# Performance work log

Hardware: AMD Instinct MI355X
Metric: run time of the kernel (lower is better)

## Reference

```python
import jax, jax.numpy as jnp
from jax import lax
import numpy as np

TOP_K = 2
CAPACITY_FACTOR = 1.0


def setup_inputs() -> dict:
    key = jax.random.key(0)
    kx, kg, k1, k2 = jax.random.split(key, 4)
    B, S, D, F, E = 8, 4096, 512, 1024, 16
    x = jax.random.normal(kx, (B, S, D), dtype=jnp.float32)
    w_gate = jax.random.normal(kg, (D, E), dtype=jnp.float32) * 0.02
    w1 = jax.random.normal(k1, (E, D, 2 * F), dtype=jnp.float32) * 0.02
    w2 = jax.random.normal(k2, (E, F, D), dtype=jnp.float32) * 0.02
    return {"x": x, "w_gate": w_gate, "w1": w1, "w2": w2}


def reference(x, w_gate, w1, w2):
    # Inference mode: no gating noise, dropout is identity.
    B, S, D = x.shape
    E = w_gate.shape[1]
    T = B * S
    capacity = max(1, int(CAPACITY_FACTOR * T / E))  # static

    flat = x.reshape(T, D)
    gate_logits = flat @ w_gate                      # [T, E]
    gate_scores = jax.nn.softmax(gate_logits, axis=-1)
    topk_vals, topk_idx = lax.top_k(gate_scores, TOP_K)  # [T, k]

    phi_mean = gate_scores.mean(axis=0)
    aux_loss = E * jnp.sum(phi_mean * phi_mean)

    # Per-expert combine weight for every token: [E, T]
    onehot = topk_idx[None, :, :] == jnp.arange(E)[:, None, None]  # [E, T, k]
    w_et = jnp.sum(jnp.where(onehot, topk_vals[None], 0.0), axis=-1)  # [E, T]

    # Capacity truncation: keep the `capacity` highest-weight tokens per expert
    sel_w, sel_idx = lax.top_k(w_et, capacity)  # [E, C]; unrouted picks have weight 0

    xs = flat[sel_idx]                                  # [E, C, D] gather
    h = jnp.einsum('ecd,edf->ecf', xs, w1)              # [E, C, 2F]
    h1, h2 = jnp.split(h, 2, axis=-1)
    act = h1 * jax.nn.silu(h2)                          # SwiGLU
    out_e = jnp.einsum('ecf,efd->ecd', act, w2) * sel_w[..., None]  # [E, C, D]

    combined = jnp.zeros((T, D), dtype=flat.dtype).at[sel_idx.reshape(-1)].add(
        out_e.reshape(-1, D))
    return combined.reshape(B, S, D), aux_loss
```

## Files before the change

### kernel.cpp

```cpp
#include <hip/hip_runtime.h>
#include <hip/hip_bf16.h>
#include <math.h>

#define T_TOK 32768
#define D_DIM 512
#define E_EXP 16
#define F_DIM 1024
#define C_CAP 2048

typedef __attribute__((ext_vector_type(8))) __bf16 bf16x8;
typedef __attribute__((ext_vector_type(4))) float f32x4;

__device__ __forceinline__ unsigned short f2bf(float f) {
  unsigned u = __float_as_uint(f);
  u += 0x7FFFu + ((u >> 16) & 1u);
  return (unsigned short)(u >> 16);
}

__device__ __forceinline__ void gld16(const void* gptr, void* ldsptr) {
  __builtin_amdgcn_global_load_lds(
      (__attribute__((address_space(1))) void*)(void*)gptr,
      (__attribute__((address_space(3))) void*)ldsptr, 16, 0, 0);
}

__global__ void transpose_conv_kernel(const float* __restrict__ in,
                                      unsigned short* __restrict__ out,
                                      int R, int Cc) {
  __shared__ float tile[32][33];
  int e = blockIdx.z;
  int r0 = blockIdx.y * 32, c0 = blockIdx.x * 32;
  const float* pin = in + (size_t)e * R * Cc;
  unsigned short* pout = out + (size_t)e * R * Cc;
  int tx = threadIdx.x, ty = threadIdx.y;
  #pragma unroll
  for (int i = 0; i < 32; i += 8)
    tile[ty + i][tx] = pin[(size_t)(r0 + ty + i) * Cc + c0 + tx];
  __syncthreads();
  #pragma unroll
  for (int i = 0; i < 32; i += 8)
    pout[(size_t)(c0 + ty + i) * R + r0 + tx] = f2bf(tile[tx][ty + i]);
}

__global__ __launch_bounds__(256) void gate_kernel(
    const float* __restrict__ x, const float* __restrict__ wg,
    float* __restrict__ w_et, float* __restrict__ phi_sum,
    unsigned short* __restrict__ xb) {
  __shared__ float wgl[D_DIM * E_EXP];
  __shared__ float phil[E_EXP];
  int tid = threadIdx.x;
  for (int i = tid; i < D_DIM * E_EXP; i += 256) wgl[i] = wg[i];
  if (tid < E_EXP) phil[tid] = 0.f;
  __syncthreads();

  int g = tid >> 4;
  int e = tid & 15;
  int t = blockIdx.x * 16 + g;

  float acc = 0.f;
  const float* xr = x + (size_t)t * D_DIM;
  #pragma unroll 4
  for (int d = 0; d < D_DIM; d += 4) {
    float4 xv = *(const float4*)(xr + d);
    acc = fmaf(xv.x, wgl[(d + 0) * 16 + e], acc);
    acc = fmaf(xv.y, wgl[(d + 1) * 16 + e], acc);
    acc = fmaf(xv.z, wgl[(d + 2) * 16 + e], acc);
    acc = fmaf(xv.w, wgl[(d + 3) * 16 + e], acc);
  }

  unsigned short* xrow = xb + (size_t)t * D_DIM;
  #pragma unroll
  for (int j = 0; j < 8; ++j) {
    int idx = j * 16 + e;
    float4 v = *(const float4*)(xr + idx * 4);
    ushort4 o;
    o.x = f2bf(v.x); o.y = f2bf(v.y); o.z = f2bf(v.z); o.w = f2bf(v.w);
    ((ushort4*)xrow)[idx] = o;
  }

  float m = acc;
  for (int off = 8; off; off >>= 1) m = fmaxf(m, __shfl_xor(m, off));
  float p = expf(acc - m);
  float s = p;
  for (int off = 8; off; off >>= 1) s += __shfl_xor(s, off);
  float score = p / s;
  atomicAdd(&phil[e], score);

  float v1 = score; int i1 = e;
  for (int off = 8; off; off >>= 1) {
    float ov = __shfl_xor(v1, off); int oi = __shfl_xor(i1, off);
    if (ov > v1 || (ov == v1 && oi < i1)) { v1 = ov; i1 = oi; }
  }
  float sc2 = (e == i1) ? -1.f : score;
  float v2 = sc2; int i2 = e;
  for (int off = 8; off; off >>= 1) {
    float ov = __shfl_xor(v2, off); int oi = __shfl_xor(i2, off);
    if (ov > v2 || (ov == v2 && oi < i2)) { v2 = ov; i2 = oi; }
  }
  if (e == 0) {
    w_et[(size_t)i1 * T_TOK + t] = v1;
    w_et[(size_t)i2 * T_TOK + t] = v2;
  }
  __syncthreads();
  if (tid < E_EXP) atomicAdd(&phi_sum[tid], phil[tid]);
}

__global__ void aux_kernel(const float* __restrict__ phi_sum, float* __restrict__ out_aux) {
  if (threadIdx.x == 0) {
    float s = 0.f;
    for (int e = 0; e < E_EXP; ++e) {
      float pm = phi_sum[e] / (float)T_TOK;
      s += pm * pm;
    }
    *out_aux = (float)E_EXP * s;
  }
}

template<int P>
__global__ __launch_bounds__(256) void s_hist(
    const float* __restrict__ w_et, unsigned* __restrict__ hist,
    const unsigned* __restrict__ prefix, const unsigned* __restrict__ done) {
  int c = blockIdx.x, e = blockIdx.y, tid = threadIdx.x;
  if (P > 0 && done[e]) return;
  __shared__ unsigned lh[2048];
  for (int i = tid; i < 2048; i += 256) lh[i] = 0;
  __syncthreads();
  const float* w = w_et + (size_t)e * T_TOK + c * 2048;
  unsigned pfx = (P > 0) ? prefix[e] : 0u;
  #pragma unroll
  for (int i = 0; i < 8; ++i) {
    unsigned b = __float_as_uint(w[i * 256 + tid]);
    if (P == 0) { if (b) atomicAdd(&lh[b >> 21], 1u); }
    else if (P == 1) { if ((b >> 21) == (pfx >> 21)) atomicAdd(&lh[(b >> 10) & 0x7FFu], 1u); }
    else { if ((b >> 10) == (pfx >> 10)) atomicAdd(&lh[b & 0x3FFu], 1u); }
  }
  __syncthreads();
  for (int i = tid; i < 2048; i += 256)
    if (lh[i]) atomicAdd(&hist[e * 2048 + i], lh[i]);
}

template<int P>
__global__ __launch_bounds__(1024) void s_pick(
    const unsigned* __restrict__ hist, unsigned* __restrict__ prefix,
    unsigned* __restrict__ krem, unsigned* __restrict__ done) {
  int tid = threadIdx.x, lane = tid & 63, e = tid >> 6;
  if (P > 0 && done[e]) return;
  const int BPL = (P == 2) ? 16 : 32;
  const int SH = (P == 0) ? 21 : (P == 1) ? 10 : 0;
  const unsigned* h = hist + e * 2048;
  unsigned S = 0;
  for (int i = 0; i < BPL; ++i) S += h[lane * BPL + i];
  unsigned U = S;
  #pragma unroll
  for (int off = 1; off < 64; off <<= 1) {
    unsigned t = __shfl_down(U, off);
    if (lane + off < 64) U += t;
  }
  unsigned Unext = __shfl_down(U, 1);
  if (lane == 63) Unext = 0;
  unsigned k = (P == 0) ? (unsigned)C_CAP : krem[e];
  if (P == 0 && lane == 0) {
    if (U < k) { done[e] = 1; prefix[e] = 0; krem[e] = 0; }
    else done[e] = 0;
  }
  if (U >= k && Unext < k) {
    unsigned cum = Unext; int chosen = 0; unsigned knew = 0;
    for (int i = BPL - 1; i >= 0; --i) {
      unsigned hh = h[lane * BPL + i];
      if (cum + hh >= k) { chosen = lane * BPL + i; knew = k - cum; break; }
      cum += hh;
    }
    if (P == 0) prefix[e] = ((unsigned)chosen) << SH;
    else prefix[e] = prefix[e] | (((unsigned)chosen) << SH);
    krem[e] = knew;
  }
}

__global__ __launch_bounds__(256) void s_count(
    const float* __restrict__ w_et, const unsigned* __restrict__ prefix,
    unsigned* __restrict__ cnt) {
  int c = blockIdx.x, e = blockIdx.y, tid = threadIdx.x;
  unsigned thr = prefix[e];
  const uint4* up = (const uint4*)(w_et + (size_t)e * T_TOK + c * 2048 + tid * 8);
  uint4 va = up[0], vb = up[1];
  unsigned gt = 0, eq = 0;
  unsigned vals[8] = {va.x, va.y, va.z, va.w, vb.x, vb.y, vb.z, vb.w};
  #pragma unroll
  for (int i = 0; i < 8; ++i) {
    if (vals[i] > thr) gt++;
    else if (vals[i] == thr) eq++;
  }
  __shared__ unsigned sc[256];
  sc[tid] = (gt << 16) | eq;
  __syncthreads();
  for (int s = 128; s; s >>= 1) {
    if (tid < s) sc[tid] += sc[tid + s];
    __syncthreads();
  }
  if (tid == 0) cnt[e * 16 + c] = sc[0];
}

__global__ __launch_bounds__(64) void s_base(
    const unsigned* __restrict__ cnt, unsigned* __restrict__ gbase,
    unsigned* __restrict__ ebase, unsigned* __restrict__ gtt,
    unsigned* __restrict__ eqt) {
  int e = threadIdx.x;
  if (e >= 16) return;
  unsigned g = 0, q = 0;
  #pragma unroll
  for (int c = 0; c < 16; ++c) {
    unsigned p = cnt[e * 16 + c];
    gbase[e * 16 + c] = g;
    ebase[e * 16 + c] = q;
    g += p >> 16;
    q += p & 0xFFFFu;
  }
  gtt[e] = g;
  eqt[e] = (unsigned)C_CAP - g;
}

__global__ __launch_bounds__(256) void s_write(
    const float* __restrict__ w_et, const unsigned* __restrict__ prefix,
    const unsigned* __restrict__ gbase, const unsigned* __restrict__ ebase,
    const unsigned* __restrict__ gtt, const unsigned* __restrict__ eqt,
    int* __restrict__ sel_idx, float* __restrict__ sel_w) {
  int c = blockIdx.x, e = blockIdx.y, tid = threadIdx.x;
  unsigned thr = prefix[e];
  const uint4* up = (const uint4*)(w_et + (size_t)e * T_TOK + c * 2048 + tid * 8);
  uint4 va = up[0], vb = up[1];
  unsigned vals[8] = {va.x, va.y, va.z, va.w, vb.x, vb.y, vb.z, vb.w};
  unsigned gt = 0, eq = 0;
  #pragma unroll
  for (int i = 0; i < 8; ++i) {
    if (vals[i] > thr) gt++;
    else if (vals[i] == thr) eq++;
  }
  __shared__ unsigned sc[256];
  unsigned mine = (gt << 16) | eq;
  sc[tid] = mine;
  __syncthreads();
  for (int off = 1; off < 256; off <<= 1) {
    unsigned add = (tid >= off) ? sc[tid - off] : 0u;
    __syncthreads();
    sc[tid] += add;
    __syncthreads();
  }
  unsigned excl = sc[tid] - mine;
  unsigned gpos = gbase[e * 16 + c] + (excl >> 16);
  unsigned qpos = ebase[e * 16 + c] + (excl & 0xFFFFu);
  unsigned gtotal = gtt[e], eqtake = eqt[e];
  int* si = sel_idx + (size_t)e * C_CAP;
  float* sw = sel_w + (size_t)e * C_CAP;
  int tokbase = c * 2048 + tid * 8;
  #pragma unroll
  for (int i = 0; i < 8; ++i) {
    unsigned b = vals[i];
    if (b > thr) {
      si[gpos] = tokbase + i; sw[gpos] = __uint_as_float(b); gpos++;
    } else if (b == thr && qpos < eqtake) {
      si[gtotal + qpos] = tokbase + i; sw[gtotal + qpos] = __uint_as_float(b); qpos++;
    }
  }
}


#define PIPE_BARRIER() do { __builtin_amdgcn_s_barrier(); __builtin_amdgcn_sched_barrier(0); } while (0)

__global__ __launch_bounds__(256, 3) void gemm1_kernel(
    const unsigned short* __restrict__ xb,
    const unsigned short* __restrict__ w1t,
    const int* __restrict__ sel_idx,
    unsigned short* __restrict__ act) {
  __shared__ __align__(16) unsigned short As[3 * 4096];
  __shared__ __align__(16) unsigned short Bs[3 * 4096];
  int bid = (blockIdx.x & 7) * 512 + (blockIdx.x >> 3);
  int nt = bid & 15, mt = (bid >> 4) & 15, e = bid >> 8;
  int tid = threadIdx.x, lane = tid & 63, wid = tid >> 6;
  int wr = wid >> 1, wc = wid & 1;
  int cl = lane & 15, rg = lane >> 4;

  int c0 = tid, c1 = 256 + tid;
  int r0 = c0 >> 2, gk0 = (c0 & 3) ^ ((r0 >> 1) & 3);
  int r1 = c1 >> 2, gk1 = (c1 & 3) ^ ((r1 >> 1) & 3);
  int tok0 = sel_idx[e * C_CAP + mt * 128 + r0];
  int tok1 = sel_idx[e * C_CAP + mt * 128 + r1];
  const unsigned short* ag0 = xb + (size_t)tok0 * D_DIM + gk0 * 8;
  const unsigned short* ag1 = xb + (size_t)tok1 * D_DIM + gk1 * 8;
  int hcol0 = (r0 < 64) ? (nt * 64 + r0) : (F_DIM + nt * 64 + (r0 - 64));
  int hcol1 = (r1 < 64) ? (nt * 64 + r1) : (F_DIM + nt * 64 + (r1 - 64));
  const unsigned short* bg0 = w1t + ((size_t)e * 2 * F_DIM + hcol0) * D_DIM + gk0 * 8;
  const unsigned short* bg1 = w1t + ((size_t)e * 2 * F_DIM + hcol1) * D_DIM + gk1 * 8;
  char* Ab = (char*)As;
  char* Bb = (char*)Bs;

#define G1_STAGE(buf, kt) do { \
    gld16(ag0 + (kt) * 32, Ab + (buf) * 8192 + tid * 16); \
    gld16(ag1 + (kt) * 32, Ab + (buf) * 8192 + 4096 + tid * 16); \
    gld16(bg0 + (kt) * 32, Bb + (buf) * 8192 + tid * 16); \
    gld16(bg1 + (kt) * 32, Bb + (buf) * 8192 + 4096 + tid * 16); \
  } while (0)

  f32x4 zero = {0.f, 0.f, 0.f, 0.f};
  f32x4 acc[4][4];
  #pragma unroll
  for (int m = 0; m < 4; ++m)
    #pragma unroll
    for (int n = 0; n < 4; ++n) acc[m][n] = zero;

#define G1_COMPUTE(buf) do { \
    const unsigned short* Ap = As + (buf) * 4096; \
    const unsigned short* Bp = Bs + (buf) * 4096; \
    bf16x8 av[4], bv[4]; \
    _Pragma("unroll") \
    for (int m = 0; m < 4; ++m) { \
      int ra = wr * 64 + m * 16 + cl; \
      av[m] = *(const bf16x8*)&Ap[(ra * 4 + (rg ^ ((ra >> 1) & 3))) * 8]; \
    } \
    _Pragma("unroll") \
    for (int n = 0; n < 4; ++n) { \
      int rb = ((n < 2) ? (wc * 32 + n * 16) : (64 + wc * 32 + (n - 2) * 16)) + cl; \
      bv[n] = *(const bf16x8*)&Bp[(rb * 4 + (rg ^ ((rb >> 1) & 3))) * 8]; \
    } \
    _Pragma("unroll") \
    for (int m = 0; m < 4; ++m) \
      _Pragma("unroll") \
      for (int n = 0; n < 4; ++n) \
        acc[m][n] = __builtin_amdgcn_mfma_f32_16x16x32_bf16(av[m], bv[n], acc[m][n], 0, 0, 0); \
  } while (0)

  const int NK = D_DIM / 32;
  G1_STAGE(0, 0);
  G1_STAGE(1, 1);
  int bc = 0, bs = 2;
  for (int kt = 0; kt < NK - 1; ++kt) {
    asm volatile("s_waitcnt vmcnt(4)" ::: "memory");
    PIPE_BARRIER();
    if (kt + 2 < NK) { G1_STAGE(bs, kt + 2); bs = (bs == 2) ? 0 : bs + 1; }
    __builtin_amdgcn_sched_barrier(0);
    G1_COMPUTE(bc);
    bc = (bc == 2) ? 0 : bc + 1;
  }
  asm volatile("s_waitcnt vmcnt(0)" ::: "memory");
  PIPE_BARRIER();
  G1_COMPUTE(bc);

  #pragma unroll
  for (int m = 0; m < 4; ++m) {
    #pragma unroll
    for (int n = 0; n < 2; ++n) {
      #pragma unroll
      for (int r = 0; r < 4; ++r) {
        int row = mt * 128 + wr * 64 + m * 16 + rg * 4 + r;
        int col = nt * 64 + wc * 32 + n * 16 + cl;
        float h1 = acc[m][n][r];
        float h2 = acc[m][n + 2][r];
        float sg = h2 / (1.f + __expf(-h2));
        act[((size_t)e * C_CAP + row) * F_DIM + col] = f2bf(h1 * sg);
      }
    }
  }
#undef G1_STAGE
#undef G1_COMPUTE
}

__global__ __launch_bounds__(256, 3) void gemm2_kernel(
    const unsigned short* __restrict__ act,
    const unsigned short* __restrict__ w2t,
    const int* __restrict__ sel_idx,
    const float* __restrict__ sel_w,
    float* __restrict__ out) {
  __shared__ __align__(16) unsigned short As[3 * 4096];
  __shared__ __align__(16) unsigned short Bs[3 * 4096];
  int bid = (blockIdx.x & 7) * 128 + (blockIdx.x >> 3);
  int nt = bid & 3, mt = (bid >> 2) & 15, e = bid >> 6;
  int tid = threadIdx.x, lane = tid & 63, wid = tid >> 6;
  int wr = wid >> 1, wc = wid & 1;
  int cl = lane & 15, rg = lane >> 4;

  int c0 = tid, c1 = 256 + tid;
  int r0 = c0 >> 2, gk0 = (c0 & 3) ^ ((r0 >> 1) & 3);
  int r1 = c1 >> 2, gk1 = (c1 & 3) ^ ((r1 >> 1) & 3);
  const unsigned short* ag0 = act + ((size_t)e * C_CAP + mt * 128 + r0) * F_DIM + gk0 * 8;
  const unsigned short* ag1 = act + ((size_t)e * C_CAP + mt * 128 + r1) * F_DIM + gk1 * 8;
  const unsigned short* bg0 = w2t + ((size_t)e * D_DIM + nt * 128 + r0) * F_DIM + gk0 * 8;
  const unsigned short* bg1 = w2t + ((size_t)e * D_DIM + nt * 128 + r1) * F_DIM + gk1 * 8;
  char* Ab = (char*)As;
  char* Bb = (char*)Bs;

#define G2_STAGE(buf, kt) do { \
    gld16(ag0 + (kt) * 32, Ab + (buf) * 8192 + tid * 16); \
    gld16(ag1 + (kt) * 32, Ab + (buf) * 8192 + 4096 + tid * 16); \
    gld16(bg0 + (kt) * 32, Bb + (buf) * 8192 + tid * 16); \
    gld16(bg1 + (kt) * 32, Bb + (buf) * 8192 + 4096 + tid * 16); \
  } while (0)

  f32x4 zero = {0.f, 0.f, 0.f, 0.f};
  f32x4 acc[4][4];
  #pragma unroll
  for (int m = 0; m < 4; ++m)
    #pragma unroll
    for (int n = 0; n < 4; ++n) acc[m][n] = zero;

#define G2_COMPUTE(buf) do { \
    const unsigned short* Ap = As + (buf) * 4096; \
    const unsigned short* Bp = Bs + (buf) * 4096; \
    bf16x8 av[4], bv[4]; \
    _Pragma("unroll") \
    for (int m = 0; m < 4; ++m) { \
      int ra = wr * 64 + m * 16 + cl; \
      av[m] = *(const bf16x8*)&Ap[(ra * 4 + (rg ^ ((ra >> 1) & 3))) * 8]; \
    } \
    _Pragma("unroll") \
    for (int n = 0; n < 4; ++n) { \
      int rb = wc * 64 + n * 16 + cl; \
      bv[n] = *(const bf16x8*)&Bp[(rb * 4 + (rg ^ ((rb >> 1) & 3))) * 8]; \
    } \
    _Pragma("unroll") \
    for (int m = 0; m < 4; ++m) \
      _Pragma("unroll") \
      for (int n = 0; n < 4; ++n) \
        acc[m][n] = __builtin_amdgcn_mfma_f32_16x16x32_bf16(av[m], bv[n], acc[m][n], 0, 0, 0); \
  } while (0)

  const int NK = F_DIM / 32;
  G2_STAGE(0, 0);
  G2_STAGE(1, 1);
  int bc = 0, bs = 2;
  for (int kt = 0; kt < NK - 1; ++kt) {
    asm volatile("s_waitcnt vmcnt(4)" ::: "memory");
    PIPE_BARRIER();
    if (kt + 2 < NK) { G2_STAGE(bs, kt + 2); bs = (bs == 2) ? 0 : bs + 1; }
    __builtin_amdgcn_sched_barrier(0);
    G2_COMPUTE(bc);
    bc = (bc == 2) ? 0 : bc + 1;
  }
  asm volatile("s_waitcnt vmcnt(0)" ::: "memory");
  PIPE_BARRIER();
  G2_COMPUTE(bc);

  #pragma unroll
  for (int m = 0; m < 4; ++m) {
    #pragma unroll
    for (int r = 0; r < 4; ++r) {
      int slot = mt * 128 + wr * 64 + m * 16 + rg * 4 + r;
      float wgt = sel_w[e * C_CAP + slot];
      int tok = sel_idx[e * C_CAP + slot];
      float* orow = out + (size_t)tok * D_DIM;
      #pragma unroll
      for (int n = 0; n < 4; ++n) {
        int col = nt * 128 + wc * 64 + n * 16 + cl;
        atomicAdd(&orow[col], acc[m][n][r] * wgt);
      }
    }
  }
#undef G2_STAGE
#undef G2_COMPUTE
}

extern "C" void kernel_launch(void* const* d_in, const int* in_sizes, int n_in,
                              void* d_out, int out_size, void* d_ws, size_t ws_size,
                              hipStream_t stream) {
  const float* x  = (const float*)d_in[0];
  const float* wg = (const float*)d_in[1];
  const float* w1 = (const float*)d_in[2];
  const float* w2 = (const float*)d_in[3];
  float* out = (float*)d_out;

  char* ws = (char*)d_ws;
  size_t off = 0;
  auto carve = [&](size_t bytes) -> void* {
    void* p = ws + off;
    off += (bytes + 255) & ~(size_t)255;
    return p;
  };
  float* w_et            = (float*)carve((size_t)E_EXP * T_TOK * 4);
  float* phi             = (float*)carve(64);
  int* sel_i             = (int*)carve((size_t)E_EXP * C_CAP * 4);
  float* sel_wv          = (float*)carve((size_t)E_EXP * C_CAP * 4);
  unsigned short* xb     = (unsigned short*)carve((size_t)T_TOK * D_DIM * 2);
  unsigned short* w1t    = (unsigned short*)carve((size_t)E_EXP * 2 * F_DIM * D_DIM * 2);
  unsigned short* w2t    = (unsigned short*)carve((size_t)E_EXP * D_DIM * F_DIM * 2);
  unsigned short* actb   = (unsigned short*)carve((size_t)E_EXP * C_CAP * F_DIM * 2);
  unsigned* hist0        = (unsigned*)carve((size_t)E_EXP * 2048 * 4);
  unsigned* hist1        = (unsigned*)carve((size_t)E_EXP * 2048 * 4);
  unsigned* hist2        = (unsigned*)carve((size_t)E_EXP * 2048 * 4);
  unsigned* prefix       = (unsigned*)carve(64 * 4);
  unsigned* krem         = (unsigned*)carve(64 * 4);
  unsigned* done         = (unsigned*)carve(64 * 4);
  unsigned* cnt          = (unsigned*)carve(256 * 4);
  unsigned* gbase        = (unsigned*)carve(256 * 4);
  unsigned* ebase        = (unsigned*)carve(256 * 4);
  unsigned* gtt          = (unsigned*)carve(64 * 4);
  unsigned* eqt          = (unsigned*)carve(64 * 4);
  if (off > ws_size) return;

  hipMemsetAsync(w_et, 0, (size_t)E_EXP * T_TOK * 4, stream);
  hipMemsetAsync(phi, 0, 64, stream);
  hipMemsetAsync(hist0, 0, (size_t)E_EXP * 2048 * 4 * 3, stream);
  hipMemsetAsync(d_out, 0, (size_t)out_size * 4, stream);

  transpose_conv_kernel<<<dim3(2 * F_DIM / 32, D_DIM / 32, E_EXP), dim3(32, 8), 0, stream>>>(
      w1, w1t, D_DIM, 2 * F_DIM);
  transpose_conv_kernel<<<dim3(D_DIM / 32, F_DIM / 32, E_EXP), dim3(32, 8), 0, stream>>>(
      w2, w2t, F_DIM, D_DIM);
  gate_kernel<<<T_TOK / 16, 256, 0, stream>>>(x, wg, w_et, phi, xb);

  s_hist<0><<<dim3(16, 16), 256, 0, stream>>>(w_et, hist0, prefix, done);
  s_pick<0><<<1, 1024, 0, stream>>>(hist0, prefix, krem, done);
  s_hist<1><<<dim3(16, 16), 256, 0, stream>>>(w_et, hist1, prefix, done);
  s_pick<1><<<1, 1024, 0, stream>>>(hist1, prefix, krem, done);
  s_hist<2><<<dim3(16, 16), 256, 0, stream>>>(w_et, hist2, prefix, done);
  s_pick<2><<<1, 1024, 0, stream>>>(hist2, prefix, krem, done);
  s_count<<<dim3(16, 16), 256, 0, stream>>>(w_et, prefix, cnt);
  s_base<<<1, 64, 0, stream>>>(cnt, gbase, ebase, gtt, eqt);
  s_write<<<dim3(16, 16), 256, 0, stream>>>(w_et, prefix, gbase, ebase, gtt, eqt,
                                            sel_i, sel_wv);

  aux_kernel<<<1, 64, 0, stream>>>(phi, out + (size_t)T_TOK * D_DIM);
  gemm1_kernel<<<E_EXP * 16 * 16, 256, 0, stream>>>(xb, w1t, sel_i, actb);
  gemm2_kernel<<<E_EXP * 16 * 4, 256, 0, stream>>>(actb, w2t, sel_i, sel_wv, out);
}
```

Measured before the change: 336.4 us.

## Replace atomic scatter-add with per-slot outputs and token combine pass; fuse selection kernels

gemm2 now writes each expert slot's weighted output to a dense buffer that reuses the xb workspace, and a new combine kernel sums each token's slots through a token-to-slot map. This removes the float atomics into the output and the output memset. The pick step is folded into the last-arriving histogram block, s_base is folded into s_write, and the transpose writes vectorised ushort4 stores. In exchange it adds an extra 64 MB write and read of per-slot outputs plus per-token atomics in s_write. The tokmap table assumes at most two slots per token.

```diff
diff --git a/kernel.cpp b/kernel.cpp
--- a/kernel.cpp
+++ b/kernel.cpp
@@ -36,9 +36,14 @@
   for (int i = 0; i < 32; i += 8)
     tile[ty + i][tx] = pin[(size_t)(r0 + ty + i) * Cc + c0 + tx];
   __syncthreads();
-  #pragma unroll
-  for (int i = 0; i < 32; i += 8)
-    pout[(size_t)(c0 + ty + i) * R + r0 + tx] = f2bf(tile[tx][ty + i]);
+  int t = ty * 32 + tx;
+  int oc = t >> 3, og = t & 7;
+  ushort4 o;
+  o.x = f2bf(tile[og * 4 + 0][oc]);
+  o.y = f2bf(tile[og * 4 + 1][oc]);
+  o.z = f2bf(tile[og * 4 + 2][oc]);
+  o.w = f2bf(tile[og * 4 + 3][oc]);
+  *(ushort4*)&pout[(size_t)(c0 + oc) * R + r0 + og * 4] = o;
 }
 
 __global__ __launch_bounds__(256) void gate_kernel(
@@ -118,7 +123,8 @@
 template<int P>
 __global__ __launch_bounds__(256) void s_hist(
     const float* __restrict__ w_et, unsigned* __restrict__ hist,
-    const unsigned* __restrict__ prefix, const unsigned* __restrict__ done) {
+    unsigned* __restrict__ prefix, unsigned* __restrict__ krem,
+    unsigned* __restrict__ done, unsigned* __restrict__ arrive) {
   int c = blockIdx.x, e = blockIdx.y, tid = threadIdx.x;
   if (P > 0 && done[e]) return;
   __shared__ unsigned lh[2048];
@@ -136,14 +142,15 @@
   __syncthreads();
   for (int i = tid; i < 2048; i += 256)
     if (lh[i]) atomicAdd(&hist[e * 2048 + i], lh[i]);
-}
-
-template<int P>
-__global__ __launch_bounds__(1024) void s_pick(
-    const unsigned* __restrict__ hist, unsigned* __restrict__ prefix,
-    unsigned* __restrict__ krem, unsigned* __restrict__ done) {
-  int tid = threadIdx.x, lane = tid & 63, e = tid >> 6;
-  if (P > 0 && done[e]) return;
+
+  __threadfence();
+  __shared__ unsigned s_last;
+  if (tid == 0) s_last = (atomicAdd(&arrive[P * 16 + e], 1u) == 15u) ? 1u : 0u;
+  __syncthreads();
+  if (!s_last) return;
+  __threadfence();
+  if (tid >= 64) return;
+  int lane = tid;
   const int BPL = (P == 2) ? 16 : 32;
   const int SH = (P == 0) ? 21 : (P == 1) ? 10 : 0;
   const unsigned* h = hist + e * 2048;
@@ -152,8 +159,8 @@
   unsigned U = S;
   #pragma unroll
   for (int off = 1; off < 64; off <<= 1) {
-    unsigned t = __shfl_down(U, off);
-    if (lane + off < 64) U += t;
+    unsigned t2 = __shfl_down(U, off);
+    if (lane + off < 64) U += t2;
   }
   unsigned Unext = __shfl_down(U, 1);
   if (lane == 63) Unext = 0;
@@ -199,32 +206,24 @@
   if (tid == 0) cnt[e * 16 + c] = sc[0];
 }
 
-__global__ __launch_bounds__(64) void s_base(
-    const unsigned* __restrict__ cnt, unsigned* __restrict__ gbase,
-    unsigned* __restrict__ ebase, unsigned* __restrict__ gtt,
-    unsigned* __restrict__ eqt) {
-  int e = threadIdx.x;
-  if (e >= 16) return;
-  unsigned g = 0, q = 0;
-  #pragma unroll
-  for (int c = 0; c < 16; ++c) {
-    unsigned p = cnt[e * 16 + c];
-    gbase[e * 16 + c] = g;
-    ebase[e * 16 + c] = q;
-    g += p >> 16;
-    q += p & 0xFFFFu;
-  }
-  gtt[e] = g;
-  eqt[e] = (unsigned)C_CAP - g;
-}
-
 __global__ __launch_bounds__(256) void s_write(
     const float* __restrict__ w_et, const unsigned* __restrict__ prefix,
-    const unsigned* __restrict__ gbase, const unsigned* __restrict__ ebase,
-    const unsigned* __restrict__ gtt, const unsigned* __restrict__ eqt,
-    int* __restrict__ sel_idx, float* __restrict__ sel_w) {
+    const unsigned* __restrict__ cnt,
+    int* __restrict__ sel_idx, float* __restrict__ sel_w,
+    int* __restrict__ tokmap, unsigned* __restrict__ cnt_tok) {
   int c = blockIdx.x, e = blockIdx.y, tid = threadIdx.x;
   unsigned thr = prefix[e];
+  __shared__ unsigned s_gb, s_eb, s_gt, s_eq;
+  if (tid == 0) {
+    unsigned g = 0, q = 0, gb = 0, eb = 0;
+    #pragma unroll
+    for (int c2 = 0; c2 < 16; ++c2) {
+      unsigned p = cnt[e * 16 + c2];
+      if (c2 < c) { gb += p >> 16; eb += p & 0xFFFFu; }
+      g += p >> 16; q += p & 0xFFFFu;
+    }
+    s_gb = gb; s_eb = eb; s_gt = g; s_eq = (unsigned)C_CAP - g;
+  }
   const uint4* up = (const uint4*)(w_et + (size_t)e * T_TOK + c * 2048 + tid * 8);
   uint4 va = up[0], vb = up[1];
   unsigned vals[8] = {va.x, va.y, va.z, va.w, vb.x, vb.y, vb.z, vb.w};
@@ -245,19 +244,28 @@
     __syncthreads();
   }
   unsigned excl = sc[tid] - mine;
-  unsigned gpos = gbase[e * 16 + c] + (excl >> 16);
-  unsigned qpos = ebase[e * 16 + c] + (excl & 0xFFFFu);
-  unsigned gtotal = gtt[e], eqtake = eqt[e];
+  unsigned gpos = s_gb + (excl >> 16);
+  unsigned qpos = s_eb + (excl & 0xFFFFu);
+  unsigned gtotal = s_gt, eqtake = s_eq;
   int* si = sel_idx + (size_t)e * C_CAP;
   float* sw = sel_w + (size_t)e * C_CAP;
   int tokbase = c * 2048 + tid * 8;
   #pragma unroll
   for (int i = 0; i < 8; ++i) {
     unsigned b = vals[i];
+    int tok = tokbase + i;
     if (b > thr) {
-      si[gpos] = tokbase + i; sw[gpos] = __uint_as_float(b); gpos++;
+      si[gpos] = tok; sw[gpos] = __uint_as_float(b);
+      unsigned j = atomicAdd(&cnt_tok[tok], 1u);
+      tokmap[tok * 2 + j] = e * C_CAP + (int)gpos;
+      gpos++;
     } else if (b == thr && qpos < eqtake) {
-      si[gtotal + qpos] = tokbase + i; sw[gtotal + qpos] = __uint_as_float(b); qpos++;
+      si[gtotal + qpos] = tok; sw[gtotal + qpos] = __uint_as_float(b);
+      if (b != 0u) {
+        unsigned j = atomicAdd(&cnt_tok[tok], 1u);
+        tokmap[tok * 2 + j] = e * C_CAP + (int)(gtotal + qpos);
+      }
+      qpos++;
     }
   }
 }
@@ -365,9 +373,8 @@
 __global__ __launch_bounds__(256, 3) void gemm2_kernel(
     const unsigned short* __restrict__ act,
     const unsigned short* __restrict__ w2t,
-    const int* __restrict__ sel_idx,
     const float* __restrict__ sel_w,
-    float* __restrict__ out) {
+    float* __restrict__ outE) {
   __shared__ __align__(16) unsigned short As[3 * 4096];
   __shared__ __align__(16) unsigned short Bs[3 * 4096];
   int bid = (blockIdx.x & 7) * 128 + (blockIdx.x >> 3);
@@ -443,17 +450,35 @@
     for (int r = 0; r < 4; ++r) {
       int slot = mt * 128 + wr * 64 + m * 16 + rg * 4 + r;
       float wgt = sel_w[e * C_CAP + slot];
-      int tok = sel_idx[e * C_CAP + slot];
-      float* orow = out + (size_t)tok * D_DIM;
+      float* orow = outE + ((size_t)e * C_CAP + slot) * D_DIM;
       #pragma unroll
       for (int n = 0; n < 4; ++n) {
         int col = nt * 128 + wc * 64 + n * 16 + cl;
-        atomicAdd(&orow[col], acc[m][n][r] * wgt);
+        orow[col] = acc[m][n][r] * wgt;
       }
     }
   }
 #undef G2_STAGE
 #undef G2_COMPUTE
+}
+
+__global__ __launch_bounds__(256) void combine_kernel(
+    const float* __restrict__ outE, const int* __restrict__ tokmap,
+    const unsigned* __restrict__ cnt_tok, float* __restrict__ out) {
+  int t = blockIdx.x * 4 + (threadIdx.x >> 6);
+  int lane = threadIdx.x & 63;
+  unsigned cnt = cnt_tok[t];
+  float4 a0 = {0.f, 0.f, 0.f, 0.f}, a1 = {0.f, 0.f, 0.f, 0.f};
+  for (unsigned j = 0; j < cnt; ++j) {
+    int s = tokmap[t * 2 + j];
+    const float4* p = (const float4*)(outE + (size_t)s * D_DIM);
+    float4 v0 = p[lane], v1 = p[lane + 64];
+    a0.x += v0.x; a0.y += v0.y; a0.z += v0.z; a0.w += v0.w;
+    a1.x += v1.x; a1.y += v1.y; a1.z += v1.z; a1.w += v1.w;
+  }
+  float4* o = (float4*)(out + (size_t)t * D_DIM);
+  o[lane] = a0;
+  o[lane + 64] = a1;
 }
 
 extern "C" void kernel_launch(void* const* d_in, const int* in_sizes, int n_in,
@@ -487,16 +512,18 @@
   unsigned* krem         = (unsigned*)carve(64 * 4);
   unsigned* done         = (unsigned*)carve(64 * 4);
   unsigned* cnt          = (unsigned*)carve(256 * 4);
-  unsigned* gbase        = (unsigned*)carve(256 * 4);
-  unsigned* ebase        = (unsigned*)carve(256 * 4);
-  unsigned* gtt          = (unsigned*)carve(64 * 4);
-  unsigned* eqt          = (unsigned*)carve(64 * 4);
+  unsigned* arrive       = (unsigned*)carve(64 * 4);
+  int* tokmap            = (int*)carve((size_t)T_TOK * 2 * 4);
+  unsigned* cnt_tok      = (unsigned*)carve((size_t)T_TOK * 4);
   if (off > ws_size) return;
+
+  float* outE = (float*)xb;
 
   hipMemsetAsync(w_et, 0, (size_t)E_EXP * T_TOK * 4, stream);
   hipMemsetAsync(phi, 0, 64, stream);
   hipMemsetAsync(hist0, 0, (size_t)E_EXP * 2048 * 4 * 3, stream);
-  hipMemsetAsync(d_out, 0, (size_t)out_size * 4, stream);
+  hipMemsetAsync(arrive, 0, 64 * 4, stream);
+  hipMemsetAsync(cnt_tok, 0, (size_t)T_TOK * 4, stream);
 
   transpose_conv_kernel<<<dim3(2 * F_DIM / 32, D_DIM / 32, E_EXP), dim3(32, 8), 0, stream>>>(
       w1, w1t, D_DIM, 2 * F_DIM);
@@ -504,18 +531,15 @@
       w2, w2t, F_DIM, D_DIM);
   gate_kernel<<<T_TOK / 16, 256, 0, stream>>>(x, wg, w_et, phi, xb);
 
-  s_hist<0><<<dim3(16, 16), 256, 0, stream>>>(w_et, hist0, prefix, done);
-  s_pick<0><<<1, 1024, 0, stream>>>(hist0, prefix, krem, done);
-  s_hist<1><<<dim3(16, 16), 256, 0, stream>>>(w_et, hist1, prefix, done);
-  s_pick<1><<<1, 1024, 0, stream>>>(hist1, prefix, krem, done);
-  s_hist<2><<<dim3(16, 16), 256, 0, stream>>>(w_et, hist2, prefix, done);
-  s_pick<2><<<1, 1024, 0, stream>>>(hist2, prefix, krem, done);
+  s_hist<0><<<dim3(16, 16), 256, 0, stream>>>(w_et, hist0, prefix, krem, done, arrive);
+  s_hist<1><<<dim3(16, 16), 256, 0, stream>>>(w_et, hist1, prefix, krem, done, arrive);
+  s_hist<2><<<dim3(16, 16), 256, 0, stream>>>(w_et, hist2, prefix, krem, done, arrive);
   s_count<<<dim3(16, 16), 256, 0, stream>>>(w_et, prefix, cnt);
-  s_base<<<1, 64, 0, stream>>>(cnt, gbase, ebase, gtt, eqt);
-  s_write<<<dim3(16, 16), 256, 0, stream>>>(w_et, prefix, gbase, ebase, gtt, eqt,
-                                            sel_i, sel_wv);
+  s_write<<<dim3(16, 16), 256, 0, stream>>>(w_et, prefix, cnt, sel_i, sel_wv,
+                                            tokmap, cnt_tok);
 
   aux_kernel<<<1, 64, 0, stream>>>(phi, out + (size_t)T_TOK * D_DIM);
   gemm1_kernel<<<E_EXP * 16 * 16, 256, 0, stream>>>(xb, w1t, sel_i, actb);
-  gemm2_kernel<<<E_EXP * 16 * 4, 256, 0, stream>>>(actb, w2t, sel_i, sel_wv, out);
-}
+  gemm2_kernel<<<E_EXP * 16 * 4, 256, 0, stream>>>(actb, w2t, sel_wv, outE);
+  combine_kernel<<<T_TOK / 4, 256, 0, stream>>>(outE, tokmap, cnt_tok, out);
+}
```

Result: slower. 347.3 us (+3.3%).
